# Optimization experiments

Hardware: AMD Instinct MI355X
Metric: run time of the kernel (lower is better)

The kernel has to match this reference:

```python
import jax, jax.numpy as jnp
import numpy as np

EMBED_DIM = 1024
NUM_HEADS = 16
HEAD_DIM = EMBED_DIM // NUM_HEADS


def setup_inputs() -> dict:
    key = jax.random.key(0)
    k1, k2, k3, k4 = jax.random.split(key, 4)
    B, N, D = 4, 2048, EMBED_DIM
    x = jax.random.normal(k1, (B, N, D), dtype=jnp.float32)
    # torch nn.Linear layout: weight [out_features, in_features]
    w_qkv = jax.random.normal(k2, (3 * D, D), dtype=jnp.float32) * (1.0 / np.sqrt(D))
    w_out = jax.random.normal(k3, (D, D), dtype=jnp.float32) * (1.0 / np.sqrt(D))
    b_out = jax.random.normal(k4, (D,), dtype=jnp.float32) * 0.01
    return {"x": x, "w_qkv": w_qkv, "w_out": w_out, "b_out": b_out}


def reference(x, w_qkv, w_out, b_out):
    B, N, D = x.shape
    H, Hd = NUM_HEADS, HEAD_DIM
    qkv = (x @ w_qkv.T).reshape(B, N, 3, H, Hd)
    q, k, v = qkv[:, :, 0], qkv[:, :, 1], qkv[:, :, 2]  # [B,N,H,Hd]
    # NOTE: contracts over BOTH heads and head_dim -> single shared [B,N,N] map
    scores = jnp.einsum('bnhd,bmhd->bnm', q, k) / np.sqrt(Hd).astype(np.float32)
    attn = jax.nn.softmax(scores, axis=-1)
    out = jnp.einsum('bnm,bmhd->bnhd', attn, v).reshape(B, N, D)
    return out @ w_out.T + b_out
```

## Files before the change

### kernel.cpp

```cpp
#include <hip/hip_runtime.h>


typedef __bf16 bf16;
typedef __attribute__((ext_vector_type(8))) __bf16 bf16x8;
typedef __attribute__((ext_vector_type(4))) __bf16 bf16x4;
typedef __attribute__((ext_vector_type(4))) float f32x4;

#define BATCH 4
#define NTOK  2048
#define DIM   1024
#define MROWS (BATCH * NTOK)
#define QKVC  (3 * DIM)

__device__ __forceinline__ void async16(const bf16* g, bf16* l) {
  __builtin_amdgcn_global_load_lds(
      (const __attribute__((address_space(1))) void*)g,
      (__attribute__((address_space(3))) void*)l, 16, 0, 0);
}

__device__ __forceinline__ void cvt4(const float* in, bf16* out, int i4) {
  float4 f = *(const float4*)(in + i4 * 4);
  bf16x4 o;
  o.x = (bf16)f.x; o.y = (bf16)f.y; o.z = (bf16)f.z; o.w = (bf16)f.w;
  *(bf16x4*)(out + i4 * 4) = o;
}

__global__ void prep(const float* __restrict__ x, const float* __restrict__ wqkv,
                     const float* __restrict__ wout,
                     bf16* __restrict__ Xbf, bf16* __restrict__ Wqkvb,
                     bf16* __restrict__ Woutb, float* __restrict__ L) {
  const int nx = MROWS * DIM / 4, nq = QKVC * DIM / 4, nw = DIM * DIM / 4;
  const int nl = BATCH * NTOK / 4;
  int i = blockIdx.x * blockDim.x + threadIdx.x;
  if (i < nx) cvt4(x, Xbf, i);
  else if (i < nx + nq) cvt4(wqkv, Wqkvb, i - nx);
  else if (i < nx + nq + nw) cvt4(wout, Woutb, i - nx - nq);
  else if (i < nx + nq + nw + nl) {
    float4 z = {0.f, 0.f, 0.f, 0.f};
    *(float4*)(L + (i - nx - nq - nw) * 4) = z;
  }
}

struct GemmCore {
  const bf16 *ga[4], *gb[4];
  int sIdx[4];
  int wm, wn, l15, kq;
};

__device__ __forceinline__ GemmCore gemm_setup(const bf16* A, const bf16* Bm,
                                               int lda, int ldb,
                                               long rowA, long rowB) {
  GemmCore g;
  const int tid = threadIdx.x;
  const int wave = tid >> 6, lane = tid & 63;
  g.wm = (wave >> 1) << 6;
  g.wn = (wave & 1) << 6;
  g.l15 = lane & 15;
  g.kq  = lane >> 4;
  const int srow = tid >> 3;
  const int sc   = tid & 7;
  const int scol = (sc ^ (srow & 7)) << 3;
#pragma unroll
  for (int seg = 0; seg < 4; ++seg) {
    g.ga[seg] = A  + (rowA + srow + 32 * seg) * (long)lda + scol;
    g.gb[seg] = Bm + (rowB + srow + 32 * seg) * (long)ldb + scol;
    g.sIdx[seg] = (srow + 32 * seg) * 64 + sc * 8;
  }
  return g;
}

__device__ __forceinline__ void gemm_kloop(const GemmCore& g, int K,
                                           bf16* As, bf16* Bs, f32x4 acc[4][4]) {
  const int sw = g.l15 & 7;
  for (int kt = 0; kt < K; kt += 64) {
#pragma unroll
    for (int seg = 0; seg < 4; ++seg) {
      async16(g.ga[seg] + kt, As + g.sIdx[seg]);
      async16(g.gb[seg] + kt, Bs + g.sIdx[seg]);
    }
    __syncthreads();

#pragma unroll
    for (int ks = 0; ks < 2; ++ks) {
      const int slot = ((ks * 4 + g.kq) ^ sw) * 8;
      bf16x8 af[4], bfm[4];
#pragma unroll
      for (int ti = 0; ti < 4; ++ti)
        af[ti] = *(const bf16x8*)&As[(g.wm + ti * 16 + g.l15) * 64 + slot];
#pragma unroll
      for (int tj = 0; tj < 4; ++tj)
        bfm[tj] = *(const bf16x8*)&Bs[(g.wn + tj * 16 + g.l15) * 64 + slot];
#pragma unroll
      for (int ti = 0; ti < 4; ++ti)
#pragma unroll
        for (int tj = 0; tj < 4; ++tj)
          acc[ti][tj] = __builtin_amdgcn_mfma_f32_16x16x32_bf16(
              af[ti], bfm[tj], acc[ti][tj], 0, 0, 0);
    }

    __syncthreads();
  }
}

template <int MODE>
__launch_bounds__(256)
__global__ void gemm_bt(const bf16* __restrict__ Aroot, const bf16* __restrict__ Broot,
                        void* __restrict__ Croot, const float* __restrict__ bias,
                        const float* __restrict__ Lroot,
                        int K, int lda, int ldb, int ldc,
                        long strideA, long strideB, long strideC) {
  const bf16* A  = Aroot + (long)blockIdx.z * strideA;
  const bf16* Bm = Broot + (long)blockIdx.z * strideB;
  __shared__ alignas(16) bf16 As[128 * 64];
  __shared__ alignas(16) bf16 Bs[128 * 64];

  const long rowA = (long)blockIdx.y * 128;
  const long rowB = (long)blockIdx.x * 128;
  GemmCore g = gemm_setup(A, Bm, lda, ldb, rowA, rowB);

  f32x4 acc[4][4] = {};
  gemm_kloop(g, K, As, Bs, acc);

  if constexpr (MODE == 0) {
    bf16* C = (bf16*)Croot + (long)blockIdx.z * strideC;
#pragma unroll
    for (int ti = 0; ti < 4; ++ti)
#pragma unroll
      for (int tj = 0; tj < 4; ++tj) {
        const long col = rowB + g.wn + tj * 16 + g.l15;
#pragma unroll
        for (int r = 0; r < 4; ++r) {
          const long row = rowA + g.wm + ti * 16 + g.kq * 4 + r;
          C[row * (long)ldc + col] = (bf16)acc[ti][tj][r];
        }
      }
  } else {
    float* C = (float*)Croot + (long)blockIdx.z * strideC;
    const float* L = Lroot + (long)blockIdx.z * NTOK;
#pragma unroll
    for (int ti = 0; ti < 4; ++ti) {
#pragma unroll
      for (int r = 0; r < 4; ++r) {
        const long row = rowA + g.wm + ti * 16 + g.kq * 4 + r;
        const float inv = 1.0f / L[row];
#pragma unroll
        for (int tj = 0; tj < 4; ++tj) {
          const long col = rowB + g.wn + tj * 16 + g.l15;
          C[row * (long)ldc + col] = acc[ti][tj][r] * inv + bias[col];
        }
      }
    }
  }
}

__launch_bounds__(256)
__global__ void gemm_sv(const bf16* __restrict__ QKV, const bf16* __restrict__ Wout,
                        bf16* __restrict__ E, bf16* __restrict__ Vpp,
                        float* __restrict__ Lroot) {
  __shared__ alignas(16) bf16 As[128 * 64];
  __shared__ alignas(16) bf16 Bs[128 * 64];

  const int z = blockIdx.z;
  if (z < 4) {
    const bf16* A  = QKV + (long)z * NTOK * QKVC;
    const bf16* Bm = A + DIM;
    const long rowA = (long)blockIdx.y * 128;
    const long rowB = (long)blockIdx.x * 128;
    GemmCore g = gemm_setup(A, Bm, QKVC, QKVC, rowA, rowB);
    f32x4 acc[4][4] = {};
    gemm_kloop(g, DIM, As, Bs, acc);

    bf16* C = E + (long)z * NTOK * NTOK;
    float* L = Lroot + (long)z * NTOK;
#pragma unroll
    for (int ti = 0; ti < 4; ++ti) {
#pragma unroll
      for (int r = 0; r < 4; ++r) {
        const long row = rowA + g.wm + ti * 16 + g.kq * 4 + r;
        float psum = 0.f;
#pragma unroll
        for (int tj = 0; tj < 4; ++tj) {
          const long col = rowB + g.wn + tj * 16 + g.l15;
          float e = __expf(acc[ti][tj][r] * 0.125f);
          bf16 eb = (bf16)e;
          C[row * (long)NTOK + col] = eb;
          psum += (float)eb;
        }
#pragma unroll
        for (int off = 8; off >= 1; off >>= 1) psum += __shfl_xor(psum, off, 64);
        if (g.l15 == 0) atomicAdd(&L[row], psum);
      }
    }
  } else {
    if (blockIdx.y >= 8) return;
    const int b = z - 4;
    const bf16* Bm = QKV + (long)b * NTOK * QKVC + 2 * DIM;
    const long rowA = (long)blockIdx.y * 128;
    const long rowB = (long)blockIdx.x * 128;
    GemmCore g = gemm_setup(Wout, Bm, DIM, QKVC, rowA, rowB);
    f32x4 acc[4][4] = {};
    gemm_kloop(g, DIM, As, Bs, acc);

    bf16* C = Vpp + (long)b * DIM * NTOK;
#pragma unroll
    for (int ti = 0; ti < 4; ++ti)
#pragma unroll
      for (int tj = 0; tj < 4; ++tj) {
        const long col = rowB + g.wn + tj * 16 + g.l15;
#pragma unroll
        for (int r = 0; r < 4; ++r) {
          const long row = rowA + g.wm + ti * 16 + g.kq * 4 + r;
          C[row * (long)NTOK + col] = (bf16)acc[ti][tj][r];
        }
      }
  }
}

extern "C" void kernel_launch(void* const* d_in, const int* in_sizes, int n_in,
                              void* d_out, int out_size, void* d_ws, size_t ws_size,
                              hipStream_t stream) {
  const float* x      = (const float*)d_in[0];
  const float* w_qkv  = (const float*)d_in[1];
  const float* w_out  = (const float*)d_in[2];
  const float* b_out  = (const float*)d_in[3];
  float* out = (float*)d_out;

  char* w = (char*)d_ws;
  bf16*  Xbf   = (bf16*)(w);
  bf16*  Wqkvb = (bf16*)(w + 16777216);
  bf16*  Woutb = (bf16*)(w + 23068672);
  bf16*  QKV   = (bf16*)(w + 25165824);
  bf16*  E     = (bf16*)(w + 75497472);
  bf16*  Vpp   = (bf16*)(w + 109051904);
  float* L     = (float*)(w + 125829120);

  {
    const int n4 = MROWS * DIM / 4 + QKVC * DIM / 4 + DIM * DIM / 4 + BATCH * NTOK / 4;
    prep<<<(n4 + 255) / 256, 256, 0, stream>>>(x, w_qkv, w_out, Xbf, Wqkvb, Woutb, L);
  }

  gemm_bt<0><<<dim3(QKVC / 128, MROWS / 128, 1), 256, 0, stream>>>(
      Xbf, Wqkvb, QKV, nullptr, nullptr, DIM, DIM, DIM, QKVC, 0, 0, 0);

  gemm_sv<<<dim3(NTOK / 128, NTOK / 128, 2 * BATCH), 256, 0, stream>>>(
      QKV, Woutb, E, Vpp, L);

  gemm_bt<2><<<dim3(DIM / 128, NTOK / 128, BATCH), 256, 0, stream>>>(
      E, Vpp, out, b_out, L, NTOK, NTOK, NTOK, DIM,
      (long)NTOK * NTOK, (long)DIM * NTOK, (long)NTOK * DIM);
}
```

Measured before the change: 277.2 us.

## Double-buffer LDS and use 32x32x16 MFMA in QKV and output GEMMs

The gemm_bt kernel, used for the QKV projection and the final attention-times-V' GEMM, now uses two LDS buffers. The async global-to-LDS load of the next K tile is issued before the MFMAs on the current tile, with one barrier per tile. It also switches from 16x16x32 to 32x32x16 bf16 MFMA tiles, which changes the fragment loads and the epilogue row mapping. The aim is to hide global load latency behind compute and cut barrier and LDS read overhead. The cost is twice the LDS per block (64 KB), which may lower occupancy. The scores kernel gemm_sv still uses the old single-buffer 16x16 path.

```diff
diff --git a/kernel.cpp b/kernel.cpp
--- a/kernel.cpp
+++ b/kernel.cpp
@@ -4,6 +4,7 @@
 typedef __bf16 bf16;
 typedef __attribute__((ext_vector_type(8))) __bf16 bf16x8;
 typedef __attribute__((ext_vector_type(4))) __bf16 bf16x4;
+typedef __attribute__((ext_vector_type(16))) float f32x16;
 typedef __attribute__((ext_vector_type(4))) float f32x4;
 
 #define BATCH 4
@@ -41,16 +42,159 @@
   }
 }
 
-struct GemmCore {
+struct Core32 {
+  const bf16 *ga[4], *gb[4];
+  int sIdx[4];
+  int wm, wn, l31, half;
+};
+
+__device__ __forceinline__ Core32 c32_setup(const bf16* A, const bf16* Bm,
+                                            int lda, int ldb,
+                                            long rowA, long rowB) {
+  Core32 g;
+  const int tid = threadIdx.x;
+  const int wave = tid >> 6, lane = tid & 63;
+  g.wm = (wave >> 1) << 6;
+  g.wn = (wave & 1) << 6;
+  g.l31 = lane & 31;
+  g.half = lane >> 5;
+  const int srow = tid >> 3;
+  const int sc   = tid & 7;
+  const int scol = (sc ^ (srow & 7)) << 3;
+#pragma unroll
+  for (int seg = 0; seg < 4; ++seg) {
+    g.ga[seg] = A  + (rowA + srow + 32 * seg) * (long)lda + scol;
+    g.gb[seg] = Bm + (rowB + srow + 32 * seg) * (long)ldb + scol;
+    g.sIdx[seg] = (srow + 32 * seg) * 64 + sc * 8;
+  }
+  return g;
+}
+
+__device__ __forceinline__ void c32_stage(const Core32& g, int kt,
+                                          bf16* As, bf16* Bs) {
+#pragma unroll
+  for (int seg = 0; seg < 4; ++seg) {
+    async16(g.ga[seg] + kt, As + g.sIdx[seg]);
+    async16(g.gb[seg] + kt, Bs + g.sIdx[seg]);
+  }
+}
+
+__device__ __forceinline__ void c32_compute(const Core32& g,
+                                            const bf16* As, const bf16* Bs,
+                                            f32x16 acc[2][2]) {
+  const int sw = g.l31 & 7;
+  bf16x8 af[2][4], bfm[2][4];
+#pragma unroll
+  for (int ti = 0; ti < 2; ++ti)
+#pragma unroll
+    for (int s = 0; s < 4; ++s)
+      af[ti][s] = *(const bf16x8*)&As[(g.wm + ti * 32 + g.l31) * 64 + ((s * 2 + g.half) ^ sw) * 8];
+#pragma unroll
+  for (int tj = 0; tj < 2; ++tj)
+#pragma unroll
+    for (int s = 0; s < 4; ++s)
+      bfm[tj][s] = *(const bf16x8*)&Bs[(g.wn + tj * 32 + g.l31) * 64 + ((s * 2 + g.half) ^ sw) * 8];
+
+#pragma unroll
+  for (int s = 0; s < 4; ++s)
+#pragma unroll
+    for (int ti = 0; ti < 2; ++ti)
+#pragma unroll
+      for (int tj = 0; tj < 2; ++tj)
+        acc[ti][tj] = __builtin_amdgcn_mfma_f32_32x32x16_bf16(
+            af[ti][s], bfm[tj][s], acc[ti][tj], 0, 0, 0);
+}
+
+__device__ __forceinline__ void c32_sync() {
+  asm volatile("s_waitcnt vmcnt(0) lgkmcnt(0)" ::: "memory");
+  __builtin_amdgcn_s_barrier();
+}
+
+__device__ __forceinline__ void c32_kloop(const Core32& g, int K,
+                                          bf16* As0, bf16* Bs0,
+                                          bf16* As1, bf16* Bs1,
+                                          f32x16 acc[2][2]) {
+  c32_stage(g, 0, As0, Bs0);
+  c32_sync();
+  const int nt = K >> 6;
+#pragma unroll 1
+  for (int t2 = 0; t2 < nt / 2 - 1; ++t2) {
+    c32_stage(g, (2 * t2 + 1) * 64, As1, Bs1);
+    c32_compute(g, As0, Bs0, acc);
+    c32_sync();
+    c32_stage(g, (2 * t2 + 2) * 64, As0, Bs0);
+    c32_compute(g, As1, Bs1, acc);
+    c32_sync();
+  }
+  c32_stage(g, (nt - 1) * 64, As1, Bs1);
+  c32_compute(g, As0, Bs0, acc);
+  c32_sync();
+  c32_compute(g, As1, Bs1, acc);
+}
+
+template <int MODE>
+__launch_bounds__(256)
+__global__ void gemm_bt(const bf16* __restrict__ Aroot, const bf16* __restrict__ Broot,
+                        void* __restrict__ Croot, const float* __restrict__ bias,
+                        const float* __restrict__ Lroot,
+                        int K, int lda, int ldb, int ldc,
+                        long strideA, long strideB, long strideC) {
+  const bf16* A  = Aroot + (long)blockIdx.z * strideA;
+  const bf16* Bm = Broot + (long)blockIdx.z * strideB;
+  __shared__ alignas(16) bf16 As0[128 * 64];
+  __shared__ alignas(16) bf16 Bs0[128 * 64];
+  __shared__ alignas(16) bf16 As1[128 * 64];
+  __shared__ alignas(16) bf16 Bs1[128 * 64];
+
+  const long rowA = (long)blockIdx.y * 128;
+  const long rowB = (long)blockIdx.x * 128;
+  Core32 g = c32_setup(A, Bm, lda, ldb, rowA, rowB);
+
+  f32x16 acc[2][2] = {};
+  c32_kloop(g, K, As0, Bs0, As1, Bs1, acc);
+
+  if constexpr (MODE == 0) {
+    bf16* C = (bf16*)Croot + (long)blockIdx.z * strideC;
+#pragma unroll
+    for (int ti = 0; ti < 2; ++ti)
+#pragma unroll
+      for (int tj = 0; tj < 2; ++tj) {
+        const long col = rowB + g.wn + tj * 32 + g.l31;
+#pragma unroll
+        for (int r = 0; r < 16; ++r) {
+          const long row = rowA + g.wm + ti * 32 + (r & 3) + 8 * (r >> 2) + 4 * g.half;
+          C[row * (long)ldc + col] = (bf16)acc[ti][tj][r];
+        }
+      }
+  } else {
+    float* C = (float*)Croot + (long)blockIdx.z * strideC;
+    const float* L = Lroot + (long)blockIdx.z * NTOK;
+#pragma unroll
+    for (int ti = 0; ti < 2; ++ti) {
+#pragma unroll
+      for (int r = 0; r < 16; ++r) {
+        const long row = rowA + g.wm + ti * 32 + (r & 3) + 8 * (r >> 2) + 4 * g.half;
+        const float inv = 1.0f / L[row];
+#pragma unroll
+        for (int tj = 0; tj < 2; ++tj) {
+          const long col = rowB + g.wn + tj * 32 + g.l31;
+          C[row * (long)ldc + col] = acc[ti][tj][r] * inv + bias[col];
+        }
+      }
+    }
+  }
+}
+
+struct Core16 {
   const bf16 *ga[4], *gb[4];
   int sIdx[4];
   int wm, wn, l15, kq;
 };
 
-__device__ __forceinline__ GemmCore gemm_setup(const bf16* A, const bf16* Bm,
-                                               int lda, int ldb,
-                                               long rowA, long rowB) {
-  GemmCore g;
+__device__ __forceinline__ Core16 c16_setup(const bf16* A, const bf16* Bm,
+                                            int lda, int ldb,
+                                            long rowA, long rowB) {
+  Core16 g;
   const int tid = threadIdx.x;
   const int wave = tid >> 6, lane = tid & 63;
   g.wm = (wave >> 1) << 6;
@@ -69,8 +213,8 @@
   return g;
 }
 
-__device__ __forceinline__ void gemm_kloop(const GemmCore& g, int K,
-                                           bf16* As, bf16* Bs, f32x4 acc[4][4]) {
+__device__ __forceinline__ void c16_kloop(const Core16& g, int K,
+                                          bf16* As, bf16* Bs, f32x4 acc[4][4]) {
   const int sw = g.l15 & 7;
   for (int kt = 0; kt < K; kt += 64) {
 #pragma unroll
@@ -99,57 +243,6 @@
     }
 
     __syncthreads();
-  }
-}
-
-template <int MODE>
-__launch_bounds__(256)
-__global__ void gemm_bt(const bf16* __restrict__ Aroot, const bf16* __restrict__ Broot,
-                        void* __restrict__ Croot, const float* __restrict__ bias,
-                        const float* __restrict__ Lroot,
-                        int K, int lda, int ldb, int ldc,
-                        long strideA, long strideB, long strideC) {
-  const bf16* A  = Aroot + (long)blockIdx.z * strideA;
-  const bf16* Bm = Broot + (long)blockIdx.z * strideB;
-  __shared__ alignas(16) bf16 As[128 * 64];
-  __shared__ alignas(16) bf16 Bs[128 * 64];
-
-  const long rowA = (long)blockIdx.y * 128;
-  const long rowB = (long)blockIdx.x * 128;
-  GemmCore g = gemm_setup(A, Bm, lda, ldb, rowA, rowB);
-
-  f32x4 acc[4][4] = {};
-  gemm_kloop(g, K, As, Bs, acc);
-
-  if constexpr (MODE == 0) {
-    bf16* C = (bf16*)Croot + (long)blockIdx.z * strideC;
-#pragma unroll
-    for (int ti = 0; ti < 4; ++ti)
-#pragma unroll
-      for (int tj = 0; tj < 4; ++tj) {
-        const long col = rowB + g.wn + tj * 16 + g.l15;
-#pragma unroll
-        for (int r = 0; r < 4; ++r) {
-          const long row = rowA + g.wm + ti * 16 + g.kq * 4 + r;
-          C[row * (long)ldc + col] = (bf16)acc[ti][tj][r];
-        }
-      }
-  } else {
-    float* C = (float*)Croot + (long)blockIdx.z * strideC;
-    const float* L = Lroot + (long)blockIdx.z * NTOK;
-#pragma unroll
-    for (int ti = 0; ti < 4; ++ti) {
-#pragma unroll
-      for (int r = 0; r < 4; ++r) {
-        const long row = rowA + g.wm + ti * 16 + g.kq * 4 + r;
-        const float inv = 1.0f / L[row];
-#pragma unroll
-        for (int tj = 0; tj < 4; ++tj) {
-          const long col = rowB + g.wn + tj * 16 + g.l15;
-          C[row * (long)ldc + col] = acc[ti][tj][r] * inv + bias[col];
-        }
-      }
-    }
   }
 }
 
@@ -166,9 +259,9 @@
     const bf16* Bm = A + DIM;
     const long rowA = (long)blockIdx.y * 128;
     const long rowB = (long)blockIdx.x * 128;
-    GemmCore g = gemm_setup(A, Bm, QKVC, QKVC, rowA, rowB);
+    Core16 g = c16_setup(A, Bm, QKVC, QKVC, rowA, rowB);
     f32x4 acc[4][4] = {};
-    gemm_kloop(g, DIM, As, Bs, acc);
+    c16_kloop(g, DIM, As, Bs, acc);
 
     bf16* C = E + (long)z * NTOK * NTOK;
     float* L = Lroot + (long)z * NTOK;
@@ -197,9 +290,9 @@
     const bf16* Bm = QKV + (long)b * NTOK * QKVC + 2 * DIM;
     const long rowA = (long)blockIdx.y * 128;
     const long rowB = (long)blockIdx.x * 128;
-    GemmCore g = gemm_setup(Wout, Bm, DIM, QKVC, rowA, rowB);
+    Core16 g = c16_setup(Wout, Bm, DIM, QKVC, rowA, rowB);
     f32x4 acc[4][4] = {};
-    gemm_kloop(g, DIM, As, Bs, acc);
+    c16_kloop(g, DIM, As, Bs, acc);
 
     bf16* C = Vpp + (long)b * DIM * NTOK;
 #pragma unroll
```

New measurement: 265.2 us, median of 5. 1.05x faster.
